# Kernel optimization log

Measured on AMD Instinct MI355X. Metric: run time of the kernel, lower is better.

## Reference

```python
import jax, jax.numpy as jnp
import numpy as np

SM_SCALE = 0.08838834764831845  # 1/sqrt(128)
Q_LEN, K_LEN, H, M, D = 1024, 1024, 8, 8, 128


def setup_inputs() -> dict:
    key = jax.random.key(0)
    k1, k2, k3, k4 = jax.random.split(key, 4)
    Q = jax.random.normal(k1, (Q_LEN, H, M, D), dtype=jnp.float32)
    K_expanded = jax.random.normal(k2, (K_LEN, H, M, D), dtype=jnp.float32)
    mask = jax.random.normal(k3, (Q_LEN, K_LEN), dtype=jnp.float32)
    sinks = jax.random.normal(k4, (H, M, Q_LEN, 1), dtype=jnp.float32)
    return {"Q": Q, "K_expanded": K_expanded, "mask": mask, "sinks": sinks}


def reference(Q, K_expanded, mask, sinks):
    # [h, m, q, k] scaled scores + additive mask
    QK = jnp.einsum('qhmd,khmd->hmqk', Q, K_expanded) * SM_SCALE
    QK = QK + mask[None, None, :, :]
    # append sink logits on the key axis -> [h, m, q, k+1]
    return jnp.concatenate([QK, sinks], axis=-1)
```

## Files before the change

kernel.cpp:

```cpp
#include <hip/hip_runtime.h>
#include <hip/hip_bf16.h>
#include <stdint.h>

#define QL 1024
#define KL 1024
#define HM 64
#define DD 128
#define SM_SCALE 0.08838834764831845f
#define LDP 136

typedef __bf16 bf16x8 __attribute__((ext_vector_type(8)));
typedef __bf16 bf16x4 __attribute__((ext_vector_type(4)));
typedef float floatx4 __attribute__((ext_vector_type(4)));

__global__ __launch_bounds__(256, 2)
void qk3_kernel(const float* __restrict__ Qg, const float* __restrict__ Kg,
                const float* __restrict__ mask, const float* __restrict__ sinks,
                float* __restrict__ out)
{
    const int bid   = blockIdx.x;
    const int xcd   = bid & 7;
    const int inner = bid >> 3;
    const int qt    = inner & 7;
    const int g     = xcd * 8 + (inner >> 3);

    __shared__ __bf16 Qs[128][LDP];
    __shared__ __bf16 Ks[2][64][LDP];

    const int t = threadIdx.x;

    const float* Qbase = Qg + (size_t)(qt * 128) * (HM * DD) + (size_t)g * DD;
    const float* Kbase = Kg + (size_t)g * DD;
#pragma unroll
    for (int j = 0; j < 16; ++j) {
        int c = t + 256 * j;
        int row = c >> 5, c4 = c & 31;
        float4 a = *(const float4*)(Qbase + (size_t)row * (HM * DD) + c4 * 4);
        bf16x4 av = { (__bf16)a.x, (__bf16)a.y, (__bf16)a.z, (__bf16)a.w };
        *(bf16x4*)&Qs[row][c4 * 4] = av;
    }
#pragma unroll
    for (int j = 0; j < 8; ++j) {
        int c = t + 256 * j;
        int row = c >> 5, c4 = c & 31;
        float4 b = *(const float4*)(Kbase + (size_t)row * (HM * DD) + c4 * 4);
        bf16x4 bv = { (__bf16)b.x, (__bf16)b.y, (__bf16)b.z, (__bf16)b.w };
        *(bf16x4*)&Ks[0][row][c4 * 4] = bv;
    }
    __syncthreads();

    const int wave = t >> 6;
    const int lane = t & 63;
    const int wm   = (wave & 1) * 64;
    const int wnk  = (wave >> 1) * 32;
    const int lr   = lane & 15;
    const int quad = lane >> 4;

    const size_t obase = (size_t)g * QL * 1025;

    for (int kt = 0; kt < 16; ++kt) {
        const int b = kt & 1;

        float4 nf[8];
        if (kt < 15) {
            const float* nb = Kg + (size_t)((kt + 1) * 64) * (HM * DD) + (size_t)g * DD;
#pragma unroll
            for (int j = 0; j < 8; ++j) {
                int c = t + 256 * j;
                nf[j] = *(const float4*)(nb + (size_t)(c >> 5) * (HM * DD) + (c & 31) * 4);
            }
        }

        floatx4 acc[4][2] = {};
#pragma unroll
        for (int ks = 0; ks < 4; ++ks) {
            const int d0 = ks * 32 + quad * 8;
            bf16x8 af[4], bfr[2];
#pragma unroll
            for (int mi = 0; mi < 4; ++mi)
                af[mi] = *(const bf16x8*)&Qs[wm + mi * 16 + lr][d0];
#pragma unroll
            for (int ni = 0; ni < 2; ++ni)
                bfr[ni] = *(const bf16x8*)&Ks[b][wnk + ni * 16 + lr][d0];
#pragma unroll
            for (int mi = 0; mi < 4; ++mi)
#pragma unroll
                for (int ni = 0; ni < 2; ++ni)
                    acc[mi][ni] = __builtin_amdgcn_mfma_f32_16x16x32_bf16(
                        bfr[ni], af[mi], acc[mi][ni], 0, 0, 0);
        }

#pragma unroll
        for (int mi = 0; mi < 4; ++mi) {
            const int q = (qt << 7) + wm + mi * 16 + lr;
            const float* mrow = mask + ((size_t)q << 10);
            float* orow = out + obase + (size_t)q * 1025;
#pragma unroll
            for (int ni = 0; ni < 2; ++ni) {
                const int k0 = (kt << 6) + wnk + ni * 16 + (quad << 2);
                floatx4 mv = *(const floatx4*)(mrow + k0);
                floatx4 v  = acc[mi][ni] * SM_SCALE + mv;
                __builtin_memcpy((void*)(orow + k0), &v, 16);
            }
        }

        if (kt < 15) {
#pragma unroll
            for (int j = 0; j < 8; ++j) {
                int c = t + 256 * j;
                bf16x4 bv = { (__bf16)nf[j].x, (__bf16)nf[j].y,
                              (__bf16)nf[j].z, (__bf16)nf[j].w };
                *(bf16x4*)&Ks[1 - b][c >> 5][(c & 31) * 4] = bv;
            }
            __syncthreads();
        }
    }

    if (t < 128) {
        const int q = (qt << 7) + t;
        out[obase + (size_t)q * 1025 + 1024] = sinks[((size_t)g << 10) + q];
    }
}

extern "C" void kernel_launch(void* const* d_in, const int* in_sizes, int n_in,
                              void* d_out, int out_size, void* d_ws, size_t ws_size,
                              hipStream_t stream)
{
    const float* Q     = (const float*)d_in[0];
    const float* K     = (const float*)d_in[1];
    const float* mask  = (const float*)d_in[2];
    const float* sinks = (const float*)d_in[3];
    float* out = (float*)d_out;

    qk3_kernel<<<512, 256, 0, stream>>>(Q, K, mask, sinks, out);
}
```

Measured before the change: 418.7 us.

## Load Q/K fragments directly into registers, drop LDS staging, use nontemporal stores

Removes shared-memory staging and the double-buffered K pipeline. Each wave now loads its own Q fragments into registers once and reads K fragments straight from global memory every k-tile, converting to bf16 in registers. This removes LDS traffic and the block-wide barriers. The cost is redundant global K loads across waves and no prefetch overlap. Output stores become nontemporal so the large write stream bypasses the cache.

```diff
diff --git a/kernel.cpp b/kernel.cpp
--- a/kernel.cpp
+++ b/kernel.cpp
@@ -7,14 +7,13 @@
 #define HM 64
 #define DD 128
 #define SM_SCALE 0.08838834764831845f
-#define LDP 136
 
 typedef __bf16 bf16x8 __attribute__((ext_vector_type(8)));
-typedef __bf16 bf16x4 __attribute__((ext_vector_type(4)));
 typedef float floatx4 __attribute__((ext_vector_type(4)));
+typedef float floatx4u __attribute__((ext_vector_type(4), aligned(4)));
 
 __global__ __launch_bounds__(256, 2)
-void qk3_kernel(const float* __restrict__ Qg, const float* __restrict__ Kg,
+void qk4_kernel(const float* __restrict__ Qg, const float* __restrict__ Kg,
                 const float* __restrict__ mask, const float* __restrict__ sinks,
                 float* __restrict__ out)
 {
@@ -24,31 +23,7 @@
     const int qt    = inner & 7;
     const int g     = xcd * 8 + (inner >> 3);
 
-    __shared__ __bf16 Qs[128][LDP];
-    __shared__ __bf16 Ks[2][64][LDP];
-
-    const int t = threadIdx.x;
-
-    const float* Qbase = Qg + (size_t)(qt * 128) * (HM * DD) + (size_t)g * DD;
-    const float* Kbase = Kg + (size_t)g * DD;
-#pragma unroll
-    for (int j = 0; j < 16; ++j) {
-        int c = t + 256 * j;
-        int row = c >> 5, c4 = c & 31;
-        float4 a = *(const float4*)(Qbase + (size_t)row * (HM * DD) + c4 * 4);
-        bf16x4 av = { (__bf16)a.x, (__bf16)a.y, (__bf16)a.z, (__bf16)a.w };
-        *(bf16x4*)&Qs[row][c4 * 4] = av;
-    }
-#pragma unroll
-    for (int j = 0; j < 8; ++j) {
-        int c = t + 256 * j;
-        int row = c >> 5, c4 = c & 31;
-        float4 b = *(const float4*)(Kbase + (size_t)row * (HM * DD) + c4 * 4);
-        bf16x4 bv = { (__bf16)b.x, (__bf16)b.y, (__bf16)b.z, (__bf16)b.w };
-        *(bf16x4*)&Ks[0][row][c4 * 4] = bv;
-    }
-    __syncthreads();
-
+    const int t    = threadIdx.x;
     const int wave = t >> 6;
     const int lane = t & 63;
     const int wm   = (wave & 1) * 64;
@@ -56,39 +31,49 @@
     const int lr   = lane & 15;
     const int quad = lane >> 4;
 
+    bf16x8 af[4][4];
+    {
+        const float* Qb = Qg + ((size_t)(qt * 128 + wm + lr) * HM + g) * DD + quad * 8;
+#pragma unroll
+        for (int mi = 0; mi < 4; ++mi) {
+            const float* qr = Qb + (size_t)mi * 16 * HM * DD;
+#pragma unroll
+            for (int ks = 0; ks < 4; ++ks) {
+                float4 a = *(const float4*)(qr + ks * 32);
+                float4 b = *(const float4*)(qr + ks * 32 + 4);
+                af[ks][mi] = (bf16x8){ (__bf16)a.x, (__bf16)a.y, (__bf16)a.z, (__bf16)a.w,
+                                       (__bf16)b.x, (__bf16)b.y, (__bf16)b.z, (__bf16)b.w };
+            }
+        }
+    }
+
     const size_t obase = (size_t)g * QL * 1025;
+    const float* Kb0 = Kg + ((size_t)(wnk + lr) * HM + g) * DD + quad * 8;
 
     for (int kt = 0; kt < 16; ++kt) {
-        const int b = kt & 1;
-
-        float4 nf[8];
-        if (kt < 15) {
-            const float* nb = Kg + (size_t)((kt + 1) * 64) * (HM * DD) + (size_t)g * DD;
+        const float* Kb = Kb0 + (size_t)(kt * 64) * (HM * DD);
+        bf16x8 bfr[4][2];
 #pragma unroll
-            for (int j = 0; j < 8; ++j) {
-                int c = t + 256 * j;
-                nf[j] = *(const float4*)(nb + (size_t)(c >> 5) * (HM * DD) + (c & 31) * 4);
+        for (int ni = 0; ni < 2; ++ni) {
+            const float* kr = Kb + (size_t)ni * 16 * (HM * DD);
+#pragma unroll
+            for (int ks = 0; ks < 4; ++ks) {
+                float4 x = *(const float4*)(kr + ks * 32);
+                float4 y = *(const float4*)(kr + ks * 32 + 4);
+                bfr[ks][ni] = (bf16x8){ (__bf16)x.x, (__bf16)x.y, (__bf16)x.z, (__bf16)x.w,
+                                        (__bf16)y.x, (__bf16)y.y, (__bf16)y.z, (__bf16)y.w };
             }
         }
 
         floatx4 acc[4][2] = {};
 #pragma unroll
-        for (int ks = 0; ks < 4; ++ks) {
-            const int d0 = ks * 32 + quad * 8;
-            bf16x8 af[4], bfr[2];
-#pragma unroll
-            for (int mi = 0; mi < 4; ++mi)
-                af[mi] = *(const bf16x8*)&Qs[wm + mi * 16 + lr][d0];
-#pragma unroll
-            for (int ni = 0; ni < 2; ++ni)
-                bfr[ni] = *(const bf16x8*)&Ks[b][wnk + ni * 16 + lr][d0];
+        for (int ks = 0; ks < 4; ++ks)
 #pragma unroll
             for (int mi = 0; mi < 4; ++mi)
 #pragma unroll
                 for (int ni = 0; ni < 2; ++ni)
                     acc[mi][ni] = __builtin_amdgcn_mfma_f32_16x16x32_bf16(
-                        bfr[ni], af[mi], acc[mi][ni], 0, 0, 0);
-        }
+                        bfr[ks][ni], af[ks][mi], acc[mi][ni], 0, 0, 0);
 
 #pragma unroll
         for (int mi = 0; mi < 4; ++mi) {
@@ -100,19 +85,8 @@
                 const int k0 = (kt << 6) + wnk + ni * 16 + (quad << 2);
                 floatx4 mv = *(const floatx4*)(mrow + k0);
                 floatx4 v  = acc[mi][ni] * SM_SCALE + mv;
-                __builtin_memcpy((void*)(orow + k0), &v, 16);
+                __builtin_nontemporal_store(v, (floatx4u*)(orow + k0));
             }
-        }
-
-        if (kt < 15) {
-#pragma unroll
-            for (int j = 0; j < 8; ++j) {
-                int c = t + 256 * j;
-                bf16x4 bv = { (__bf16)nf[j].x, (__bf16)nf[j].y,
-                              (__bf16)nf[j].z, (__bf16)nf[j].w };
-                *(bf16x4*)&Ks[1 - b][c >> 5][(c & 31) * 4] = bv;
-            }
-            __syncthreads();
         }
     }
 
@@ -132,5 +106,5 @@
     const float* sinks = (const float*)d_in[3];
     float* out = (float*)d_out;
 
-    qk3_kernel<<<512, 256, 0, stream>>>(Q, K, mask, sinks, out);
+    qk4_kernel<<<512, 256, 0, stream>>>(Q, K, mask, sinks, out);
 }
```

After: 523.6 us. 25.1% more time.

## Keep Q fragments in registers and stage output through LDS for coalesced stores

Applied to the files above, without the earlier changes.

Q fragments are now loaded straight from global memory into registers, and the Q shared-memory tile is removed. Each wave now covers 32 query rows against the full 64-key tile instead of a 64x32 split. Accumulators are written to a per-wave shared-memory staging buffer and read back row-contiguously, so mask loads and output stores span full 64-float row segments instead of scattered 16-byte pieces. This aims to improve global coalescing on a store-heavy kernel, at the cost of extra LDS traffic, more registers and more shared memory per block.

```diff
diff --git a/kernel.cpp b/kernel.cpp
--- a/kernel.cpp
+++ b/kernel.cpp
@@ -8,13 +8,15 @@
 #define DD 128
 #define SM_SCALE 0.08838834764831845f
 #define LDP 136
+#define OSP 68
 
 typedef __bf16 bf16x8 __attribute__((ext_vector_type(8)));
 typedef __bf16 bf16x4 __attribute__((ext_vector_type(4)));
 typedef float floatx4 __attribute__((ext_vector_type(4)));
+typedef float floatx4u __attribute__((ext_vector_type(4), aligned(4)));
 
 __global__ __launch_bounds__(256, 2)
-void qk3_kernel(const float* __restrict__ Qg, const float* __restrict__ Kg,
+void qk6_kernel(const float* __restrict__ Qg, const float* __restrict__ Kg,
                 const float* __restrict__ mask, const float* __restrict__ sinks,
                 float* __restrict__ out)
 {
@@ -24,21 +26,33 @@
     const int qt    = inner & 7;
     const int g     = xcd * 8 + (inner >> 3);
 
-    __shared__ __bf16 Qs[128][LDP];
     __shared__ __bf16 Ks[2][64][LDP];
+    __shared__ float  Os[4][32][OSP];
 
-    const int t = threadIdx.x;
+    const int t    = threadIdx.x;
+    const int wave = t >> 6;
+    const int lane = t & 63;
+    const int lr   = lane & 15;
+    const int quad = lane >> 4;
+    const int wm   = wave * 32;
 
-    const float* Qbase = Qg + (size_t)(qt * 128) * (HM * DD) + (size_t)g * DD;
+    bf16x8 af[4][2];
+    {
+        const float* Qb = Qg + ((size_t)(qt * 128 + wm + lr) * HM + g) * DD + quad * 8;
+#pragma unroll
+        for (int mi = 0; mi < 2; ++mi) {
+            const float* qr = Qb + (size_t)mi * 16 * HM * DD;
+#pragma unroll
+            for (int ks = 0; ks < 4; ++ks) {
+                float4 a = *(const float4*)(qr + ks * 32);
+                float4 b = *(const float4*)(qr + ks * 32 + 4);
+                af[ks][mi] = (bf16x8){ (__bf16)a.x, (__bf16)a.y, (__bf16)a.z, (__bf16)a.w,
+                                       (__bf16)b.x, (__bf16)b.y, (__bf16)b.z, (__bf16)b.w };
+            }
+        }
+    }
+
     const float* Kbase = Kg + (size_t)g * DD;
-#pragma unroll
-    for (int j = 0; j < 16; ++j) {
-        int c = t + 256 * j;
-        int row = c >> 5, c4 = c & 31;
-        float4 a = *(const float4*)(Qbase + (size_t)row * (HM * DD) + c4 * 4);
-        bf16x4 av = { (__bf16)a.x, (__bf16)a.y, (__bf16)a.z, (__bf16)a.w };
-        *(bf16x4*)&Qs[row][c4 * 4] = av;
-    }
 #pragma unroll
     for (int j = 0; j < 8; ++j) {
         int c = t + 256 * j;
@@ -48,13 +62,6 @@
         *(bf16x4*)&Ks[0][row][c4 * 4] = bv;
     }
     __syncthreads();
-
-    const int wave = t >> 6;
-    const int lane = t & 63;
-    const int wm   = (wave & 1) * 64;
-    const int wnk  = (wave >> 1) * 32;
-    const int lr   = lane & 15;
-    const int quad = lane >> 4;
 
     const size_t obase = (size_t)g * QL * 1025;
 
@@ -71,37 +78,38 @@
             }
         }
 
-        floatx4 acc[4][2] = {};
+        floatx4 acc[2][4] = {};
 #pragma unroll
         for (int ks = 0; ks < 4; ++ks) {
             const int d0 = ks * 32 + quad * 8;
-            bf16x8 af[4], bfr[2];
+            bf16x8 kf[4];
 #pragma unroll
-            for (int mi = 0; mi < 4; ++mi)
-                af[mi] = *(const bf16x8*)&Qs[wm + mi * 16 + lr][d0];
+            for (int ni = 0; ni < 4; ++ni)
+                kf[ni] = *(const bf16x8*)&Ks[b][ni * 16 + lr][d0];
 #pragma unroll
-            for (int ni = 0; ni < 2; ++ni)
-                bfr[ni] = *(const bf16x8*)&Ks[b][wnk + ni * 16 + lr][d0];
+            for (int mi = 0; mi < 2; ++mi)
 #pragma unroll
-            for (int mi = 0; mi < 4; ++mi)
-#pragma unroll
-                for (int ni = 0; ni < 2; ++ni)
+                for (int ni = 0; ni < 4; ++ni)
                     acc[mi][ni] = __builtin_amdgcn_mfma_f32_16x16x32_bf16(
-                        bfr[ni], af[mi], acc[mi][ni], 0, 0, 0);
+                        kf[ni], af[ks][mi], acc[mi][ni], 0, 0, 0);
         }
 
 #pragma unroll
-        for (int mi = 0; mi < 4; ++mi) {
-            const int q = (qt << 7) + wm + mi * 16 + lr;
-            const float* mrow = mask + ((size_t)q << 10);
-            float* orow = out + obase + (size_t)q * 1025;
+        for (int mi = 0; mi < 2; ++mi)
 #pragma unroll
-            for (int ni = 0; ni < 2; ++ni) {
-                const int k0 = (kt << 6) + wnk + ni * 16 + (quad << 2);
-                floatx4 mv = *(const floatx4*)(mrow + k0);
-                floatx4 v  = acc[mi][ni] * SM_SCALE + mv;
-                __builtin_memcpy((void*)(orow + k0), &v, 16);
-            }
+            for (int ni = 0; ni < 4; ++ni)
+                *(floatx4*)&Os[wave][mi * 16 + lr][ni * 16 + quad * 4] = acc[mi][ni];
+
+#pragma unroll
+        for (int j = 0; j < 8; ++j) {
+            int c = lane + 64 * j;
+            int row = c >> 4, col = (c & 15) * 4;
+            floatx4 v = *(const floatx4*)&Os[wave][row][col];
+            const int q = (qt << 7) + wm + row;
+            const int k0 = (kt << 6) + col;
+            floatx4 mv = *(const floatx4*)(mask + ((size_t)q << 10) + k0);
+            v = v * SM_SCALE + mv;
+            *(floatx4u*)(out + obase + (size_t)q * 1025 + k0) = v;
         }
 
         if (kt < 15) {
@@ -132,5 +140,5 @@
     const float* sinks = (const float*)d_in[3];
     float* out = (float*)d_out;
 
-    qk3_kernel<<<512, 256, 0, stream>>>(Q, K, mask, sinks, out);
+    qk6_kernel<<<512, 256, 0, stream>>>(Q, K, mask, sinks, out);
 }
```

Measured after the change: 398.7 us. -4.8%, faster.
